# Kernel optimization log

Measured on AMD Instinct MI355X. Metric: run time of the kernel, lower is better.

## Reference

```python
import jax, jax.numpy as jnp
import numpy as np

K_CURV = 1.0   # Lorentz(k=1.0)
EPS = 1e-6


def _project(space):
    # lift space components onto hyperboloid: t = sqrt(k + ||s||^2)
    t = jnp.sqrt(K_CURV + jnp.sum(space * space, axis=-1, keepdims=True))
    return jnp.concatenate([t, space], axis=-1)


def setup_inputs():
    key = jax.random.key(0)
    B, N, D, H = 4, 1024, 128, 8
    ks = jax.random.split(key, 7)
    # valid Lorentz points: [B, N, D] with x[...,0] the time coordinate
    x = _project(jax.random.normal(ks[0], (B, N, D - 1), dtype=jnp.float32) * 0.5)
    scale = 1.0 / np.sqrt(D)
    Wq = jax.random.normal(ks[1], (H, D - 1, D), dtype=jnp.float32) * scale
    Wk = jax.random.normal(ks[2], (H, D - 1, D), dtype=jnp.float32) * scale
    Wv = jax.random.normal(ks[3], (H, D - 1, D), dtype=jnp.float32) * scale
    bq = jnp.zeros((H, D - 1), dtype=jnp.float32)
    bk = jnp.zeros((H, D - 1), dtype=jnp.float32)
    bv = jnp.zeros((H, D - 1), dtype=jnp.float32)
    beta = jnp.ones((H,), dtype=jnp.float32)
    gamma = jnp.zeros((H,), dtype=jnp.float32)
    return {"x": x, "Wq": Wq, "bq": bq, "Wk": Wk, "bk": bk, "Wv": Wv, "bv": bv,
            "beta": beta, "gamma": gamma}


def _lorentz_fc(x, W, b):
    # HyboNet-style Lorentz fully-connected (identity activation), all heads at once.
    # x: [B,N,D], W: [H,D-1,D], b: [H,D-1] -> [H,B,N,D] on the hyperboloid
    space = jnp.einsum('bnd,hed->hbne', x, W) + b[:, None, None, :]
    return _project(space)


def reference(x, Wq, bq, Wk, bk, Wv, bv, beta, gamma):
    D = x.shape[-1]
    sign = jnp.concatenate([-jnp.ones((1,), x.dtype), jnp.ones((D - 1,), x.dtype)])
    Q = _lorentz_fc(x, Wq, bq)   # [H,B,N,D]
    K = _lorentz_fc(x, Wk, bk)
    V = _lorentz_fc(x, Wv, bv)
    # pairwise Minkowski inner product <q,k>_L = -t_q t_k + s_q . s_k
    inner = jnp.einsum('hbid,hbjd->hbij', Q * sign, K)          # [H,B,N,N]
    dists = jnp.arccosh(jnp.maximum(-inner / K_CURV, 1.0 + EPS)) * np.sqrt(K_CURV)
    scores = -beta[:, None, None, None] * dists - gamma[:, None, None, None]
    attn = jax.nn.softmax(scores, axis=-1)
    # Lorentz midpoint: normalize weighted sum back onto the hyperboloid
    mid = jnp.einsum('hbij,hbjd->hbid', attn, V)                # [H,B,N,D]
    mnorm = jnp.einsum('hbid,hbid->hbi', mid * sign, mid)       # <m,m>_L (negative)
    head_out = mid * (np.sqrt(K_CURV) / jnp.sqrt(jnp.maximum(-mnorm, EPS)))[..., None]
    # direct_concat: concatenate space parts, recompute time coordinate
    H = head_out.shape[0]
    t = head_out[..., 0]                                        # [H,B,N]
    s = jnp.moveaxis(head_out[..., 1:], 0, 2)                   # [B,N,H,D-1]
    space_cat = s.reshape(s.shape[0], s.shape[1], -1)           # [B,N,H*(D-1)]
    time = jnp.sqrt(jnp.maximum(jnp.sum(t * t, axis=0) - (H - 1) * K_CURV, EPS))
    return jnp.concatenate([time[..., None], space_cat], axis=-1)  # [B,N,H*(D-1)+1]
```

## Files before the change

kernel.cpp:

```cpp
#include <hip/hip_runtime.h>

typedef __attribute__((ext_vector_type(8))) short short8_t;
typedef __attribute__((ext_vector_type(4))) short short4_t;
typedef __attribute__((ext_vector_type(4))) float float4_t;
typedef __attribute__((ext_vector_type(2))) unsigned int uint2_t;

__device__ __forceinline__ unsigned short f2bf(float f) {
    unsigned u = __builtin_bit_cast(unsigned, f);
    u += 0x7FFFu + ((u >> 16) & 1u);
    return (unsigned short)(u >> 16);
}

__device__ __forceinline__ unsigned pk_bf16(float a, float b) {
    unsigned r;
    asm("v_cvt_pk_bf16_f32 %0, %1, %2" : "=v"(r) : "v"(a), "v"(b));
    return r;
}

__device__ __forceinline__ short8_t pk8(float4_t a, float4_t b) {
    union { unsigned u[4]; short8_t s; } r;
    r.u[0] = pk_bf16(a[0], a[1]); r.u[1] = pk_bf16(a[2], a[3]);
    r.u[2] = pk_bf16(b[0], b[1]); r.u[3] = pk_bf16(b[2], b[3]);
    return r.s;
}

#define MFMA(A, B, C) __builtin_amdgcn_mfma_f32_16x16x32_bf16((A), (B), (C), 0, 0, 0)

__global__ __launch_bounds__(256, 4) void k_proj(
    const float* __restrict__ x,
    const float* __restrict__ Wq, const float* __restrict__ bq,
    const float* __restrict__ Wk, const float* __restrict__ bk,
    const float* __restrict__ Wv, const float* __restrict__ bv,
    unsigned short* __restrict__ Qs, unsigned short* __restrict__ Kb,
    unsigned short* __restrict__ Vt)
{
    __shared__ __align__(16) unsigned char lds[19456];
    unsigned short* Xs  = (unsigned short*)lds;
    unsigned short* Ot  = (unsigned short*)lds;
    unsigned short* OtT = (unsigned short*)lds;
    float*          ssqB = (float*)(lds + 18432);

    const int tid = threadIdx.x;
    const int m0  = blockIdx.x * 64;
    const int h   = blockIdx.y;
    const int mat = blockIdx.z;
    const float* W  = (mat == 0) ? Wq : ((mat == 1) ? Wk : Wv);
    const float* bb = (mat == 0) ? bq : ((mat == 1) ? bk : bv);

    const int w = tid >> 6, lane = tid & 63, li = lane & 15, lg = lane >> 4;

    const int e = w * 32 + li;
    float4_t wf[8][2];
    #pragma unroll
    for (int ni = 0; ni < 2; ni++) {
        int ee = e + ni * 16;
        const float* wp = W + (h * 127 + (ee < 127 ? ee : 0)) * 128 + lg * 8;
        #pragma unroll
        for (int kk = 0; kk < 4; kk++) {
            float4_t a = *(const float4_t*)(wp + kk * 32);
            float4_t b2 = *(const float4_t*)(wp + kk * 32 + 4);
            if (ee >= 127) { a = (float4_t){0.f,0.f,0.f,0.f}; b2 = (float4_t){0.f,0.f,0.f,0.f}; }
            wf[ni * 4 + kk][0] = a; wf[ni * 4 + kk][1] = b2;
        }
    }

    #pragma unroll
    for (int p = 0; p < 8; p++) {
        int r = p * 8 + (tid >> 5), c = (tid & 31) * 4;
        float4_t v = *(const float4_t*)(x + (m0 + r) * 128 + c);
        uint2_t u; u[0] = pk_bf16(v[0], v[1]); u[1] = pk_bf16(v[2], v[3]);
        *(uint2_t*)(Xs + r * 136 + c) = u;
    }
    __syncthreads();

    short8_t Bf[8];
    #pragma unroll
    for (int f = 0; f < 8; f++) Bf[f] = pk8(wf[f][0], wf[f][1]);

    float4_t acc[4][2];
    #pragma unroll
    for (int i = 0; i < 4; i++)
        #pragma unroll
        for (int j = 0; j < 2; j++) acc[i][j] = (float4_t){0.f, 0.f, 0.f, 0.f};

    #pragma unroll
    for (int kk = 0; kk < 4; kk++) {
        #pragma unroll
        for (int mi = 0; mi < 4; mi++) {
            short8_t A = *(short8_t*)(Xs + (mi * 16 + li) * 136 + kk * 32 + lg * 8);
            acc[mi][0] = MFMA(A, Bf[kk],     acc[mi][0]);
            acc[mi][1] = MFMA(A, Bf[4 + kk], acc[mi][1]);
        }
    }
    #pragma unroll
    for (int ni = 0; ni < 2; ni++) {
        int ee = e + ni * 16;
        float bvv = (ee < 127) ? bb[h * 127 + ee] : 0.0f;
        #pragma unroll
        for (int mi = 0; mi < 4; mi++)
            #pragma unroll
            for (int r = 0; r < 4; r++) acc[mi][ni][r] += bvv;
    }
    #pragma unroll
    for (int mi = 0; mi < 4; mi++) {
        #pragma unroll
        for (int r = 0; r < 4; r++) {
            float s = acc[mi][0][r] * acc[mi][0][r] + acc[mi][1][r] * acc[mi][1][r];
            s += __shfl_xor(s, 1);  s += __shfl_xor(s, 2);
            s += __shfl_xor(s, 4);  s += __shfl_xor(s, 8);
            if (li == 0) ssqB[(mi * 16 + lg * 4 + r) * 4 + w] = s;
        }
    }
    __syncthreads();

    if (mat < 2) {
        #pragma unroll
        for (int mi = 0; mi < 4; mi++)
            #pragma unroll
            for (int ni = 0; ni < 2; ni++) {
                int ee = e + ni * 16;
                if (ee < 127) {
                    #pragma unroll
                    for (int r = 0; r < 4; r++)
                        Ot[(mi * 16 + lg * 4 + r) * 136 + 1 + ee] = f2bf(acc[mi][ni][r]);
                }
            }
        if (tid < 64) {
            float s = ssqB[tid * 4] + ssqB[tid * 4 + 1] + ssqB[tid * 4 + 2] + ssqB[tid * 4 + 3];
            float t = sqrtf(1.0f + s);
            Ot[tid * 136] = f2bf(mat == 0 ? -t : t);
        }
        __syncthreads();
        unsigned short* dst = ((mat == 0) ? Qs : Kb) + (h * 4096 + m0) * 128;
        #pragma unroll
        for (int p = 0; p < 4; p++) {
            int r = p * 16 + (tid >> 4), c = (tid & 15) * 8;
            *(short8_t*)(dst + r * 128 + c) = *(short8_t*)(Ot + r * 136 + c);
        }
    } else {
        #pragma unroll
        for (int mi = 0; mi < 4; mi++)
            #pragma unroll
            for (int ni = 0; ni < 2; ni++) {
                int ee = e + ni * 16;
                if (ee < 127) {
                    uint2_t u;
                    u[0] = pk_bf16(acc[mi][ni][0], acc[mi][ni][1]);
                    u[1] = pk_bf16(acc[mi][ni][2], acc[mi][ni][3]);
                    *(uint2_t*)(OtT + (1 + ee) * 72 + mi * 16 + lg * 4) = u;
                }
            }
        if (tid < 64) {
            float s = ssqB[tid * 4] + ssqB[tid * 4 + 1] + ssqB[tid * 4 + 2] + ssqB[tid * 4 + 3];
            OtT[tid] = f2bf(sqrtf(1.0f + s));
        }
        __syncthreads();
        int b = m0 >> 10, n0 = m0 & 1023;
        unsigned short* dst = Vt + (h * 4 + b) * 131072 + n0;
        #pragma unroll
        for (int p = 0; p < 4; p++) {
            int d = p * 32 + (tid >> 3), nc = (tid & 7) * 8;
            *(short8_t*)(dst + d * 1024 + nc) = *(short8_t*)(OtT + d * 72 + nc);
        }
    }
}

__global__ __launch_bounds__(256, 3) void k_attn(
    const unsigned short* __restrict__ Qsg, const unsigned short* __restrict__ Kb,
    const unsigned short* __restrict__ Vt,
    const float* __restrict__ beta, const float* __restrict__ gamma,
    float* __restrict__ out, float* __restrict__ tsq)
{
    __shared__ __align__(16) unsigned char lds[45056];
    unsigned short* Ks  = (unsigned short*)lds;
    unsigned short* Vts = (unsigned short*)(lds + 17408);
    unsigned short* Ps  = (unsigned short*)(lds + 35840);
    float*          ow  = (float*)lds;

    const int tid = threadIdx.x, w = tid >> 6, lane = tid & 63;
    const int li = lane & 15, lg = lane >> 4;

    const int bid = blockIdx.x;
    const int hb = (bid & 7) * 4 + (bid >> 7);
    const int qt = (bid >> 3) & 15;
    const int h = hb >> 2, b = hb & 3;
    const int q0 = qt * 64;

    const unsigned short* Qp = Qsg + (h * 4096 + b * 1024) * 128;
    const unsigned short* Kp = Kb  + (h * 4096 + b * 1024) * 128;
    const unsigned short* Vp = Vt  + (h * 4 + b) * 131072;
    const float bet = beta[h];
    const bool beta1 = (bet == 1.0f);
    (void)gamma;

    const int kr = tid >> 4, kc = (tid & 15) * 8;
    const int vd = tid >> 3, vc = (tid & 7) * 8;
    const unsigned short* Kld = Kp + kr * 128 + kc;
    const unsigned short* Vld = Vp + vd * 1024 + vc;

    short8_t qf[4];
    const int qrow = q0 + w * 16 + li;
    #pragma unroll
    for (int kk = 0; kk < 4; kk++)
        qf[kk] = *(const short8_t*)(Qp + qrow * 128 + kk * 32 + lg * 8);

    float4_t amid[8];
    #pragma unroll
    for (int df = 0; df < 8; df++) amid[df] = (float4_t){0.f, 0.f, 0.f, 0.f};
    float m = -INFINITY, lsum = 0.0f;

    short8_t kreg[4], vreg[4];
    #pragma unroll
    for (int p = 0; p < 4; p++) {
        kreg[p] = *(const short8_t*)(Kld + p * 2048);
        vreg[p] = *(const short8_t*)(Vld + p * 32768);
    }
    #pragma unroll
    for (int p = 0; p < 4; p++) {
        *(short8_t*)(Ks  + (p * 16 + kr) * 136 + kc) = kreg[p];
        *(short8_t*)(Vts + (p * 32 + vd) * 72 + vc) = vreg[p];
    }
    __syncthreads();

    for (int t = 0; t < 16; t++) {
        if (t < 15) {
            const int j0n = (t + 1) * 64;
            #pragma unroll
            for (int p = 0; p < 4; p++) {
                kreg[p] = *(const short8_t*)(Kld + j0n * 128 + p * 2048);
                vreg[p] = *(const short8_t*)(Vld + p * 32768 + j0n);
            }
        }
        __builtin_amdgcn_sched_barrier(0);

        float4_t as[4];
        #pragma unroll
        for (int jf = 0; jf < 4; jf++) as[jf] = (float4_t){0.f, 0.f, 0.f, 0.f};
        __builtin_amdgcn_s_setprio(1);
        #pragma unroll
        for (int kk = 0; kk < 4; kk++) {
            #pragma unroll
            for (int jf = 0; jf < 4; jf++) {
                short8_t A = *(short8_t*)(Ks + (jf * 16 + li) * 136 + kk * 32 + lg * 8);
                as[jf] = MFMA(A, qf[kk], as[jf]);
            }
        }
        __builtin_amdgcn_s_setprio(0);

        float ps_ = 0.0f;
        if (beta1) {
            #pragma unroll
            for (int jf = 0; jf < 4; jf++) {
                float p[4];
                #pragma unroll
                for (int r = 0; r < 4; r++) {
                    float z = fmaxf(-as[jf][r], 1.0f + 1e-6f);
                    float wv = z + __builtin_amdgcn_sqrtf(__builtin_fmaf(z, z, -1.0f));
                    p[r] = __builtin_amdgcn_rcpf(wv);
                    ps_ += p[r];
                }
                uint2_t u; u[0] = pk_bf16(p[0], p[1]); u[1] = pk_bf16(p[2], p[3]);
                *(uint2_t*)(Ps + (w * 16 + li) * 72 + jf * 16 + lg * 4) = u;
            }
        } else {
            float s2[16];
            float tm = -INFINITY;
            #pragma unroll
            for (int jf = 0; jf < 4; jf++) {
                #pragma unroll
                for (int r = 0; r < 4; r++) {
                    float z = fmaxf(-as[jf][r], 1.0f + 1e-6f);
                    float wv = z + __builtin_amdgcn_sqrtf(__builtin_fmaf(z, z, -1.0f));
                    float s = -bet * __builtin_amdgcn_logf(wv);
                    s2[jf * 4 + r] = s;
                    tm = fmaxf(tm, s);
                }
            }
            tm = fmaxf(tm, __shfl_xor(tm, 16));
            tm = fmaxf(tm, __shfl_xor(tm, 32));
            if (__any(tm > m + 8.0f)) {
                float mn = fmaxf(m, tm);
                float scale = __builtin_amdgcn_exp2f(m - mn);
                lsum *= scale;
                #pragma unroll
                for (int df = 0; df < 8; df++)
                    #pragma unroll
                    for (int r = 0; r < 4; r++) amid[df][r] *= scale;
                m = mn;
            }
            #pragma unroll
            for (int jf = 0; jf < 4; jf++) {
                float p0 = __builtin_amdgcn_exp2f(s2[jf * 4 + 0] - m);
                float p1 = __builtin_amdgcn_exp2f(s2[jf * 4 + 1] - m);
                float p2 = __builtin_amdgcn_exp2f(s2[jf * 4 + 2] - m);
                float p3 = __builtin_amdgcn_exp2f(s2[jf * 4 + 3] - m);
                ps_ += (p0 + p1) + (p2 + p3);
                uint2_t u; u[0] = pk_bf16(p0, p1); u[1] = pk_bf16(p2, p3);
                *(uint2_t*)(Ps + (w * 16 + li) * 72 + jf * 16 + lg * 4) = u;
            }
        }
        ps_ += __shfl_xor(ps_, 16);
        ps_ += __shfl_xor(ps_, 32);
        lsum += ps_;
        asm volatile("s_waitcnt lgkmcnt(0)" ::: "memory");
        __builtin_amdgcn_sched_barrier(0);

        __builtin_amdgcn_s_setprio(1);
        #pragma unroll
        for (int kk2 = 0; kk2 < 2; kk2++) {
            short8_t Bp = *(short8_t*)(Ps + (w * 16 + li) * 72 + kk2 * 32 + lg * 8);
            #pragma unroll
            for (int df = 0; df < 8; df++) {
                short8_t A = *(short8_t*)(Vts + (df * 16 + li) * 72 + kk2 * 32 + lg * 8);
                amid[df] = MFMA(A, Bp, amid[df]);
            }
        }
        __builtin_amdgcn_s_setprio(0);

        if (t < 15) {
            __syncthreads();
            #pragma unroll
            for (int p = 0; p < 4; p++) {
                *(short8_t*)(Ks  + (p * 16 + kr) * 136 + kc) = kreg[p];
                *(short8_t*)(Vts + (p * 32 + vd) * 72 + vc) = vreg[p];
            }
            __syncthreads();
        }
    }

    float invl = 1.0f / lsum;
    float ssq = 0.0f;
    #pragma unroll
    for (int df = 0; df < 8; df++) {
        #pragma unroll
        for (int r = 0; r < 4; r++) {
            float v = amid[df][r] * invl;
            amid[df][r] = v;
            ssq += v * v;
        }
    }
    ssq += __shfl_xor(ssq, 16);
    ssq += __shfl_xor(ssq, 32);
    float tmid = __shfl(amid[0][0], li);
    float denom = fmaxf(2.0f * tmid * tmid - ssq, 1e-6f);
    float rs = 1.0f / sqrtf(denom);

    __syncthreads();
    #pragma unroll
    for (int df = 0; df < 8; df++) {
        #pragma unroll
        for (int r = 0; r < 4; r++)
            ow[w * 2112 + li * 132 + df * 16 + lg * 4 + r] = amid[df][r] * rs;
    }
    asm volatile("s_waitcnt lgkmcnt(0)" ::: "memory");
    __builtin_amdgcn_sched_barrier(0);

    #pragma unroll
    for (int i = 0; i < 16; i++) {
        int n = q0 + w * 16 + i;
        float v0 = ow[w * 2112 + i * 132 + lane];
        float v1 = ow[w * 2112 + i * 132 + 64 + lane];
        float* orow = out + (b * 1024 + n) * 1017;
        if (lane == 0) tsq[h * 4096 + b * 1024 + n] = v0 * v0;
        else           orow[h * 127 + lane] = v0;
        orow[h * 127 + 64 + lane] = v1;
    }
}

__global__ __launch_bounds__(256) void k_time(const float* __restrict__ tsq,
                                              float* __restrict__ out)
{
    int mrow = blockIdx.x * 256 + threadIdx.x;
    float s = 0.0f;
    #pragma unroll
    for (int h = 0; h < 8; h++) s += tsq[h * 4096 + mrow];
    out[mrow * 1017] = sqrtf(fmaxf(s - 7.0f, 1e-6f));
}

extern "C" void kernel_launch(void* const* d_in, const int* in_sizes, int n_in,
                              void* d_out, int out_size, void* d_ws, size_t ws_size,
                              hipStream_t stream)
{
    const float* x    = (const float*)d_in[0];
    const float* Wq   = (const float*)d_in[1];
    const float* bq   = (const float*)d_in[2];
    const float* Wk   = (const float*)d_in[3];
    const float* bk   = (const float*)d_in[4];
    const float* Wv   = (const float*)d_in[5];
    const float* bv   = (const float*)d_in[6];
    const float* beta = (const float*)d_in[7];
    const float* gam  = (const float*)d_in[8];
    float* out = (float*)d_out;

    unsigned char* ws = (unsigned char*)d_ws;
    unsigned short* Qs = (unsigned short*)(ws);
    unsigned short* Kb = (unsigned short*)(ws + 8388608);
    unsigned short* Vt = (unsigned short*)(ws + 16777216);
    float*          ts = (float*)(ws + 25165824);

    k_proj<<<dim3(64, 8, 3), 256, 0, stream>>>(x, Wq, bq, Wk, bk, Wv, bv, Qs, Kb, Vt);
    k_attn<<<dim3(512), 256, 0, stream>>>(Qs, Kb, Vt, beta, gam, out, ts);
    k_time<<<dim3(16), 256, 0, stream>>>(ts, out);
}
```

Baseline: 137.8 us.

## Split attention over key halves with partial outputs merged in separate kernel

Each attention block now handles half of the key sequence, which doubles the grid from 512 to 1024 blocks. Blocks write unnormalized partial accumulators and the running max to a workspace, and a new merge kernel combines the two halves, normalizes onto the hyperboloid and computes the time coordinate. The running sum is dropped, because the Lorentz renormalization makes the softmax denominator cancel. LDS tiles switch from padded rows to an XOR-swizzled layout, which shrinks LDS enough to raise occupancy to 4 blocks per CU, at the cost of extra partial-buffer traffic and one more launch.

```diff
diff --git a/kernel.cpp b/kernel.cpp
--- a/kernel.cpp
+++ b/kernel.cpp
@@ -165,24 +165,25 @@
     }
 }
 
-__global__ __launch_bounds__(256, 3) void k_attn(
+__global__ __launch_bounds__(256, 4) void k_attn(
     const unsigned short* __restrict__ Qsg, const unsigned short* __restrict__ Kb,
     const unsigned short* __restrict__ Vt,
     const float* __restrict__ beta, const float* __restrict__ gamma,
-    float* __restrict__ out, float* __restrict__ tsq)
+    float* __restrict__ part)
 {
-    __shared__ __align__(16) unsigned char lds[45056];
-    unsigned short* Ks  = (unsigned short*)lds;
-    unsigned short* Vts = (unsigned short*)(lds + 17408);
-    unsigned short* Ps  = (unsigned short*)(lds + 35840);
-    float*          ow  = (float*)lds;
+    __shared__ __align__(16) unsigned char lds[40960];
+    char* Kl = (char*)lds;
+    char* Vl = (char*)lds + 16384;
+    char* Pl = (char*)lds + 32768;
+    float* pw = (float*)lds;
 
     const int tid = threadIdx.x, w = tid >> 6, lane = tid & 63;
     const int li = lane & 15, lg = lane >> 4;
 
     const int bid = blockIdx.x;
-    const int hb = (bid & 7) * 4 + (bid >> 7);
-    const int qt = (bid >> 3) & 15;
+    const int hb = bid & 31;
+    const int qt = (bid >> 5) & 15;
+    const int half = (bid >> 9) & 1;
     const int h = hb >> 2, b = hb & 3;
     const int q0 = qt * 64;
 
@@ -193,10 +194,18 @@
     const bool beta1 = (bet == 1.0f);
     (void)gamma;
 
-    const int kr = tid >> 4, kc = (tid & 15) * 8;
-    const int vd = tid >> 3, vc = (tid & 7) * 8;
-    const unsigned short* Kld = Kp + kr * 128 + kc;
-    const unsigned short* Vld = Vp + vd * 1024 + vc;
+    const int kr = tid >> 4, kc16 = (tid & 15) * 16;
+    const int vd = tid >> 3, vc16 = (tid & 7) * 16;
+    const int kwb = (kr * 256 + kc16) ^ ((kr & 7) << 4);
+    const int vwb = (vd * 128 + vc16) ^ ((vd & 7) << 4);
+    const unsigned short* Kld = Kp + (half * 512 + kr) * 128 + (tid & 15) * 8;
+    const unsigned short* Vld = Vp + vd * 1024 + half * 512 + (tid & 7) * 8;
+
+    const int lxor = (li & 7) << 4;
+    const int krb = (li * 256 + lg * 16) ^ lxor;
+    const int vrb = (li * 128 + lg * 16) ^ lxor;
+    const int prb = ((w * 16 + li) * 128 + lg * 16) ^ lxor;
+    const int pwb = ((w * 16 + li) * 128 + lg * 8) ^ lxor;
 
     short8_t qf[4];
     const int qrow = q0 + w * 16 + li;
@@ -207,7 +216,7 @@
     float4_t amid[8];
     #pragma unroll
     for (int df = 0; df < 8; df++) amid[df] = (float4_t){0.f, 0.f, 0.f, 0.f};
-    float m = -INFINITY, lsum = 0.0f;
+    float m = beta1 ? 0.0f : -INFINITY;
 
     short8_t kreg[4], vreg[4];
     #pragma unroll
@@ -217,13 +226,13 @@
     }
     #pragma unroll
     for (int p = 0; p < 4; p++) {
-        *(short8_t*)(Ks  + (p * 16 + kr) * 136 + kc) = kreg[p];
-        *(short8_t*)(Vts + (p * 32 + vd) * 72 + vc) = vreg[p];
+        *(short8_t*)(Kl + p * 4096 + kwb) = kreg[p];
+        *(short8_t*)(Vl + p * 4096 + vwb) = vreg[p];
     }
     __syncthreads();
 
-    for (int t = 0; t < 16; t++) {
-        if (t < 15) {
+    for (int t = 0; t < 8; t++) {
+        if (t < 7) {
             const int j0n = (t + 1) * 64;
             #pragma unroll
             for (int p = 0; p < 4; p++) {
@@ -241,13 +250,12 @@
         for (int kk = 0; kk < 4; kk++) {
             #pragma unroll
             for (int jf = 0; jf < 4; jf++) {
-                short8_t A = *(short8_t*)(Ks + (jf * 16 + li) * 136 + kk * 32 + lg * 8);
+                short8_t A = *(short8_t*)(Kl + ((jf * 4096 + kk * 64) ^ krb));
                 as[jf] = MFMA(A, qf[kk], as[jf]);
             }
         }
         __builtin_amdgcn_s_setprio(0);
 
-        float ps_ = 0.0f;
         if (beta1) {
             #pragma unroll
             for (int jf = 0; jf < 4; jf++) {
@@ -257,10 +265,9 @@
                     float z = fmaxf(-as[jf][r], 1.0f + 1e-6f);
                     float wv = z + __builtin_amdgcn_sqrtf(__builtin_fmaf(z, z, -1.0f));
                     p[r] = __builtin_amdgcn_rcpf(wv);
-                    ps_ += p[r];
                 }
                 uint2_t u; u[0] = pk_bf16(p[0], p[1]); u[1] = pk_bf16(p[2], p[3]);
-                *(uint2_t*)(Ps + (w * 16 + li) * 72 + jf * 16 + lg * 4) = u;
+                *(uint2_t*)(Pl + ((jf * 32) ^ pwb)) = u;
             }
         } else {
             float s2[16];
@@ -281,7 +288,6 @@
             if (__any(tm > m + 8.0f)) {
                 float mn = fmaxf(m, tm);
                 float scale = __builtin_amdgcn_exp2f(m - mn);
-                lsum *= scale;
                 #pragma unroll
                 for (int df = 0; df < 8; df++)
                     #pragma unroll
@@ -294,87 +300,113 @@
                 float p1 = __builtin_amdgcn_exp2f(s2[jf * 4 + 1] - m);
                 float p2 = __builtin_amdgcn_exp2f(s2[jf * 4 + 2] - m);
                 float p3 = __builtin_amdgcn_exp2f(s2[jf * 4 + 3] - m);
-                ps_ += (p0 + p1) + (p2 + p3);
                 uint2_t u; u[0] = pk_bf16(p0, p1); u[1] = pk_bf16(p2, p3);
-                *(uint2_t*)(Ps + (w * 16 + li) * 72 + jf * 16 + lg * 4) = u;
-            }
-        }
-        ps_ += __shfl_xor(ps_, 16);
-        ps_ += __shfl_xor(ps_, 32);
-        lsum += ps_;
+                *(uint2_t*)(Pl + ((jf * 32) ^ pwb)) = u;
+            }
+        }
         asm volatile("s_waitcnt lgkmcnt(0)" ::: "memory");
         __builtin_amdgcn_sched_barrier(0);
 
         __builtin_amdgcn_s_setprio(1);
         #pragma unroll
         for (int kk2 = 0; kk2 < 2; kk2++) {
-            short8_t Bp = *(short8_t*)(Ps + (w * 16 + li) * 72 + kk2 * 32 + lg * 8);
+            short8_t Bp = *(short8_t*)(Pl + ((kk2 * 64) ^ prb));
             #pragma unroll
             for (int df = 0; df < 8; df++) {
-                short8_t A = *(short8_t*)(Vts + (df * 16 + li) * 72 + kk2 * 32 + lg * 8);
+                short8_t A = *(short8_t*)(Vl + ((df * 2048 + kk2 * 64) ^ vrb));
                 amid[df] = MFMA(A, Bp, amid[df]);
             }
         }
         __builtin_amdgcn_s_setprio(0);
 
-        if (t < 15) {
+        if (t < 7) {
             __syncthreads();
             #pragma unroll
             for (int p = 0; p < 4; p++) {
-                *(short8_t*)(Ks  + (p * 16 + kr) * 136 + kc) = kreg[p];
-                *(short8_t*)(Vts + (p * 32 + vd) * 72 + vc) = vreg[p];
+                *(short8_t*)(Kl + p * 4096 + kwb) = kreg[p];
+                *(short8_t*)(Vl + p * 4096 + vwb) = vreg[p];
             }
             __syncthreads();
         }
     }
 
-    float invl = 1.0f / lsum;
-    float ssq = 0.0f;
+    __syncthreads();
     #pragma unroll
     for (int df = 0; df < 8; df++) {
         #pragma unroll
-        for (int r = 0; r < 4; r++) {
-            float v = amid[df][r] * invl;
-            amid[df][r] = v;
-            ssq += v * v;
-        }
-    }
-    ssq += __shfl_xor(ssq, 16);
-    ssq += __shfl_xor(ssq, 32);
-    float tmid = __shfl(amid[0][0], li);
-    float denom = fmaxf(2.0f * tmid * tmid - ssq, 1e-6f);
-    float rs = 1.0f / sqrtf(denom);
-
-    __syncthreads();
-    #pragma unroll
-    for (int df = 0; df < 8; df++) {
-        #pragma unroll
         for (int r = 0; r < 4; r++)
-            ow[w * 2112 + li * 132 + df * 16 + lg * 4 + r] = amid[df][r] * rs;
-    }
+            pw[w * 2112 + li * 132 + df * 16 + lg * 4 + r] = amid[df][r];
+    }
+    if (lg == 0) pw[w * 2112 + li * 132 + 128] = m;
     asm volatile("s_waitcnt lgkmcnt(0)" ::: "memory");
     __builtin_amdgcn_sched_barrier(0);
 
-    #pragma unroll
-    for (int i = 0; i < 16; i++) {
-        int n = q0 + w * 16 + i;
-        float v0 = ow[w * 2112 + i * 132 + lane];
-        float v1 = ow[w * 2112 + i * 132 + 64 + lane];
-        float* orow = out + (b * 1024 + n) * 1017;
-        if (lane == 0) tsq[h * 4096 + b * 1024 + n] = v0 * v0;
-        else           orow[h * 127 + lane] = v0;
-        orow[h * 127 + 64 + lane] = v1;
-    }
-}
-
-__global__ __launch_bounds__(256) void k_time(const float* __restrict__ tsq,
-                                              float* __restrict__ out)
+    float* pb = part + (size_t)(((half * 8 + h) * 4 + b) * 1024 + q0 + w * 16) * 132;
+    #pragma unroll
+    for (int it = 0; it < 8; it++) {
+        int idx = it * 64 + lane;
+        int row = idx >> 5, c4 = idx & 31;
+        *(float4_t*)(pb + row * 132 + c4 * 4) =
+            *(float4_t*)(pw + w * 2112 + row * 132 + c4 * 4);
+    }
+    if (lane < 16)
+        *(float4_t*)(pb + lane * 132 + 128) =
+            *(float4_t*)(pw + w * 2112 + lane * 132 + 128);
+}
+
+__global__ __launch_bounds__(256) void k_merge(const float* __restrict__ part,
+                                               float* __restrict__ out)
 {
-    int mrow = blockIdx.x * 256 + threadIdx.x;
-    float s = 0.0f;
-    #pragma unroll
-    for (int h = 0; h < 8; h++) s += tsq[h * 4096 + mrow];
-    out[mrow * 1017] = sqrtf(fmaxf(s - 7.0f, 1e-6f));
+    const int tid = threadIdx.x, w = tid >> 6, lane = tid & 63;
+    const int h = lane >> 3, sub = lane & 7;
+    const int row = blockIdx.x * 4 + w;
+    const int b = row >> 10, n = row & 1023;
+
+    const float* p0 = part + (size_t)(((0 * 8 + h) * 4 + b) * 1024 + n) * 132;
+    const float* p1 = part + (size_t)(((1 * 8 + h) * 4 + b) * 1024 + n) * 132;
+
+    float4_t a0[4], a1[4];
+    #pragma unroll
+    for (int q = 0; q < 4; q++) {
+        a0[q] = *(const float4_t*)(p0 + sub * 16 + q * 4);
+        a1[q] = *(const float4_t*)(p1 + sub * 16 + q * 4);
+    }
+    float m0 = p0[128], m1 = p1[128];
+    float mN = fmaxf(m0, m1);
+    float s0 = __builtin_amdgcn_exp2f(m0 - mN);
+    float s1 = __builtin_amdgcn_exp2f(m1 - mN);
+
+    float4_t acc[4];
+    float ssq = 0.0f;
+    #pragma unroll
+    for (int q = 0; q < 4; q++) {
+        #pragma unroll
+        for (int e2 = 0; e2 < 4; e2++) {
+            float v = a0[q][e2] * s0 + a1[q][e2] * s1;
+            acc[q][e2] = v;
+            ssq += v * v;
+        }
+    }
+    ssq += __shfl_xor(ssq, 1);
+    ssq += __shfl_xor(ssq, 2);
+    ssq += __shfl_xor(ssq, 4);
+    float t = __shfl(acc[0][0], lane & 56);
+    float denom = fmaxf(2.0f * t * t - ssq, 1e-6f);
+    float rs = 1.0f / sqrtf(denom);
+
+    float th2 = (t * rs) * (t * rs);
+    th2 += __shfl_xor(th2, 8);
+    th2 += __shfl_xor(th2, 16);
+    th2 += __shfl_xor(th2, 32);
+    float timec = sqrtf(fmaxf(th2 - 7.0f, 1e-6f));
+
+    float* orow = out + (size_t)row * 1017;
+    if (lane == 0) orow[0] = timec;
+    #pragma unroll
+    for (int k = 0; k < 16; k++) {
+        int d = sub * 16 + k;
+        if (d > 0) orow[h * 127 + d] = acc[k >> 2][k & 3] * rs;
+    }
 }
 
 extern "C" void kernel_launch(void* const* d_in, const int* in_sizes, int n_in,
@@ -396,9 +428,9 @@
     unsigned short* Qs = (unsigned short*)(ws);
     unsigned short* Kb = (unsigned short*)(ws + 8388608);
     unsigned short* Vt = (unsigned short*)(ws + 16777216);
-    float*          ts = (float*)(ws + 25165824);
+    float*          pt = (float*)(ws + 25165824);
 
     k_proj<<<dim3(64, 8, 3), 256, 0, stream>>>(x, Wq, bq, Wk, bk, Wv, bv, Qs, Kb, Vt);
-    k_attn<<<dim3(512), 256, 0, stream>>>(Qs, Kb, Vt, beta, gam, out, ts);
-    k_time<<<dim3(16), 256, 0, stream>>>(ts, out);
-}
+    k_attn<<<dim3(1024), 256, 0, stream>>>(Qs, Kb, Vt, beta, gam, pt);
+    k_merge<<<dim3(1024), 256, 0, stream>>>(pt, out);
+}
```

Result: slower. 256.4 us (+86.0%).

## Split attention KV range across two wave groups with XOR-swizzled LDS

Applied to the files above, without the earlier changes.

The attention kernel doubles its block to 512 threads: two groups of four waves each process half of the key/value sequence for the same 64 queries, and their partial midpoint accumulators are merged through LDS at the end. The LDS tiles for K, V and P are rewritten with XOR swizzling in place of padding, to avoid bank conflicts. The running softmax sum lsum is dropped, relying on the final Lorentz normalization being scale invariant. The trade-offs are larger LDS use per block (80 KB), a merge step, and a lower clamp epsilon on the normalization denominator.

```diff
diff --git a/kernel.cpp b/kernel.cpp
--- a/kernel.cpp
+++ b/kernel.cpp
@@ -165,25 +165,25 @@
     }
 }
 
-__global__ __launch_bounds__(256, 3) void k_attn(
+__global__ __launch_bounds__(512, 4) void k_attn(
     const unsigned short* __restrict__ Qsg, const unsigned short* __restrict__ Kb,
     const unsigned short* __restrict__ Vt,
     const float* __restrict__ beta, const float* __restrict__ gamma,
     float* __restrict__ out, float* __restrict__ tsq)
 {
-    __shared__ __align__(16) unsigned char lds[45056];
-    unsigned short* Ks  = (unsigned short*)lds;
-    unsigned short* Vts = (unsigned short*)(lds + 17408);
-    unsigned short* Ps  = (unsigned short*)(lds + 35840);
-    float*          ow  = (float*)lds;
+    __shared__ __align__(16) unsigned char lds[81920];
+    char*  L   = (char*)lds;
+    float* mrg = (float*)lds;
+    float* ow  = (float*)(lds + 34816);
 
     const int tid = threadIdx.x, w = tid >> 6, lane = tid & 63;
     const int li = lane & 15, lg = lane >> 4;
+    const int qsub = w & 3, half = w >> 2;
 
     const int bid = blockIdx.x;
-    const int hb = (bid & 7) * 4 + (bid >> 7);
+    const int h = bid & 7;
     const int qt = (bid >> 3) & 15;
-    const int h = hb >> 2, b = hb & 3;
+    const int b = bid >> 7;
     const int q0 = qt * 64;
 
     const unsigned short* Qp = Qsg + (h * 4096 + b * 1024) * 128;
@@ -193,13 +193,22 @@
     const bool beta1 = (bet == 1.0f);
     (void)gamma;
 
-    const int kr = tid >> 4, kc = (tid & 15) * 8;
-    const int vd = tid >> 3, vc = (tid & 7) * 8;
-    const unsigned short* Kld = Kp + kr * 128 + kc;
-    const unsigned short* Vld = Vp + vd * 1024 + vc;
+    const int hv = tid >> 8, s = tid & 255;
+    const int kr = s >> 4, kcl = s & 15;
+    const int vd = s >> 3, vcl = s & 7;
+    const unsigned short* Kld = Kp + (hv * 512 + kr) * 128 + kcl * 8;
+    const unsigned short* Vld = Vp + vd * 1024 + hv * 512 + vcl * 8;
+    const int kwb = hv * 16384 + ((kr * 256 + kcl * 16) ^ ((kr & 7) << 4));
+    const int vwb = 32768 + hv * 16384 + ((vd * 128 + vcl * 16) ^ ((vd & 7) << 4));
+
+    const int lxor = (li & 7) << 4;
+    const int krb = half * 16384 + ((li * 256 + lg * 16) ^ lxor);
+    const int vrb = 32768 + half * 16384 + ((li * 128 + lg * 16) ^ lxor);
+    const int pwb = 65536 + w * 2048 + ((li * 128 + lg * 8) ^ lxor);
+    const int prb = 65536 + w * 2048 + ((li * 128 + lg * 16) ^ lxor);
 
     short8_t qf[4];
-    const int qrow = q0 + w * 16 + li;
+    const int qrow = q0 + qsub * 16 + li;
     #pragma unroll
     for (int kk = 0; kk < 4; kk++)
         qf[kk] = *(const short8_t*)(Qp + qrow * 128 + kk * 32 + lg * 8);
@@ -207,7 +216,7 @@
     float4_t amid[8];
     #pragma unroll
     for (int df = 0; df < 8; df++) amid[df] = (float4_t){0.f, 0.f, 0.f, 0.f};
-    float m = -INFINITY, lsum = 0.0f;
+    float m = beta1 ? 0.0f : -INFINITY;
 
     short8_t kreg[4], vreg[4];
     #pragma unroll
@@ -217,18 +226,17 @@
     }
     #pragma unroll
     for (int p = 0; p < 4; p++) {
-        *(short8_t*)(Ks  + (p * 16 + kr) * 136 + kc) = kreg[p];
-        *(short8_t*)(Vts + (p * 32 + vd) * 72 + vc) = vreg[p];
+        *(short8_t*)(L + kwb + p * 4096) = kreg[p];
+        *(short8_t*)(L + vwb + p * 4096) = vreg[p];
     }
     __syncthreads();
 
-    for (int t = 0; t < 16; t++) {
-        if (t < 15) {
-            const int j0n = (t + 1) * 64;
+    for (int t = 0; t < 8; t++) {
+        if (t < 7) {
             #pragma unroll
             for (int p = 0; p < 4; p++) {
-                kreg[p] = *(const short8_t*)(Kld + j0n * 128 + p * 2048);
-                vreg[p] = *(const short8_t*)(Vld + p * 32768 + j0n);
+                kreg[p] = *(const short8_t*)(Kld + (t + 1) * 8192 + p * 2048);
+                vreg[p] = *(const short8_t*)(Vld + p * 32768 + (t + 1) * 64);
             }
         }
         __builtin_amdgcn_sched_barrier(0);
@@ -241,13 +249,12 @@
         for (int kk = 0; kk < 4; kk++) {
             #pragma unroll
             for (int jf = 0; jf < 4; jf++) {
-                short8_t A = *(short8_t*)(Ks + (jf * 16 + li) * 136 + kk * 32 + lg * 8);
+                short8_t A = *(short8_t*)(L + ((jf * 4096 + kk * 64) ^ krb));
                 as[jf] = MFMA(A, qf[kk], as[jf]);
             }
         }
         __builtin_amdgcn_s_setprio(0);
 
-        float ps_ = 0.0f;
         if (beta1) {
             #pragma unroll
             for (int jf = 0; jf < 4; jf++) {
@@ -257,10 +264,9 @@
                     float z = fmaxf(-as[jf][r], 1.0f + 1e-6f);
                     float wv = z + __builtin_amdgcn_sqrtf(__builtin_fmaf(z, z, -1.0f));
                     p[r] = __builtin_amdgcn_rcpf(wv);
-                    ps_ += p[r];
                 }
                 uint2_t u; u[0] = pk_bf16(p[0], p[1]); u[1] = pk_bf16(p[2], p[3]);
-                *(uint2_t*)(Ps + (w * 16 + li) * 72 + jf * 16 + lg * 4) = u;
+                *(uint2_t*)(L + ((jf * 32) ^ pwb)) = u;
             }
         } else {
             float s2[16];
@@ -271,9 +277,9 @@
                 for (int r = 0; r < 4; r++) {
                     float z = fmaxf(-as[jf][r], 1.0f + 1e-6f);
                     float wv = z + __builtin_amdgcn_sqrtf(__builtin_fmaf(z, z, -1.0f));
-                    float s = -bet * __builtin_amdgcn_logf(wv);
-                    s2[jf * 4 + r] = s;
-                    tm = fmaxf(tm, s);
+                    float sc = -bet * __builtin_amdgcn_logf(wv);
+                    s2[jf * 4 + r] = sc;
+                    tm = fmaxf(tm, sc);
                 }
             }
             tm = fmaxf(tm, __shfl_xor(tm, 16));
@@ -281,7 +287,6 @@
             if (__any(tm > m + 8.0f)) {
                 float mn = fmaxf(m, tm);
                 float scale = __builtin_amdgcn_exp2f(m - mn);
-                lsum *= scale;
                 #pragma unroll
                 for (int df = 0; df < 8; df++)
                     #pragma unroll
@@ -294,72 +299,95 @@
                 float p1 = __builtin_amdgcn_exp2f(s2[jf * 4 + 1] - m);
                 float p2 = __builtin_amdgcn_exp2f(s2[jf * 4 + 2] - m);
                 float p3 = __builtin_amdgcn_exp2f(s2[jf * 4 + 3] - m);
-                ps_ += (p0 + p1) + (p2 + p3);
                 uint2_t u; u[0] = pk_bf16(p0, p1); u[1] = pk_bf16(p2, p3);
-                *(uint2_t*)(Ps + (w * 16 + li) * 72 + jf * 16 + lg * 4) = u;
-            }
-        }
-        ps_ += __shfl_xor(ps_, 16);
-        ps_ += __shfl_xor(ps_, 32);
-        lsum += ps_;
+                *(uint2_t*)(L + ((jf * 32) ^ pwb)) = u;
+            }
+        }
         asm volatile("s_waitcnt lgkmcnt(0)" ::: "memory");
         __builtin_amdgcn_sched_barrier(0);
 
         __builtin_amdgcn_s_setprio(1);
         #pragma unroll
         for (int kk2 = 0; kk2 < 2; kk2++) {
-            short8_t Bp = *(short8_t*)(Ps + (w * 16 + li) * 72 + kk2 * 32 + lg * 8);
+            short8_t Bp = *(short8_t*)(L + ((kk2 * 64) ^ prb));
             #pragma unroll
             for (int df = 0; df < 8; df++) {
-                short8_t A = *(short8_t*)(Vts + (df * 16 + li) * 72 + kk2 * 32 + lg * 8);
+                short8_t A = *(short8_t*)(L + ((df * 2048 + kk2 * 64) ^ vrb));
                 amid[df] = MFMA(A, Bp, amid[df]);
             }
         }
         __builtin_amdgcn_s_setprio(0);
 
-        if (t < 15) {
+        if (t < 7) {
             __syncthreads();
             #pragma unroll
             for (int p = 0; p < 4; p++) {
-                *(short8_t*)(Ks  + (p * 16 + kr) * 136 + kc) = kreg[p];
-                *(short8_t*)(Vts + (p * 32 + vd) * 72 + vc) = vreg[p];
+                *(short8_t*)(L + kwb + p * 4096) = kreg[p];
+                *(short8_t*)(L + vwb + p * 4096) = vreg[p];
             }
             __syncthreads();
         }
     }
 
-    float invl = 1.0f / lsum;
+    __syncthreads();
+    if (half == 1) {
+        float* mb = mrg + qsub * 2112;
+        #pragma unroll
+        for (int df = 0; df < 8; df++)
+            #pragma unroll
+            for (int r = 0; r < 4; r++)
+                mb[li * 132 + df * 16 + lg * 4 + r] = amid[df][r];
+        if (lg == 0) mb[li * 132 + 128] = m;
+    }
+    __syncthreads();
+    if (half == 1) return;
+
+    {
+        float* mb = mrg + qsub * 2112;
+        if (beta1) {
+            #pragma unroll
+            for (int df = 0; df < 8; df++)
+                #pragma unroll
+                for (int r = 0; r < 4; r++)
+                    amid[df][r] += mb[li * 132 + df * 16 + lg * 4 + r];
+        } else {
+            float m1v = mb[li * 132 + 128];
+            float mN = fmaxf(m, m1v);
+            float s0 = __builtin_amdgcn_exp2f(m - mN);
+            float s1 = __builtin_amdgcn_exp2f(m1v - mN);
+            #pragma unroll
+            for (int df = 0; df < 8; df++)
+                #pragma unroll
+                for (int r = 0; r < 4; r++)
+                    amid[df][r] = amid[df][r] * s0 + mb[li * 132 + df * 16 + lg * 4 + r] * s1;
+        }
+    }
+
     float ssq = 0.0f;
     #pragma unroll
-    for (int df = 0; df < 8; df++) {
-        #pragma unroll
-        for (int r = 0; r < 4; r++) {
-            float v = amid[df][r] * invl;
-            amid[df][r] = v;
-            ssq += v * v;
-        }
-    }
+    for (int df = 0; df < 8; df++)
+        #pragma unroll
+        for (int r = 0; r < 4; r++) ssq += amid[df][r] * amid[df][r];
     ssq += __shfl_xor(ssq, 16);
     ssq += __shfl_xor(ssq, 32);
     float tmid = __shfl(amid[0][0], li);
-    float denom = fmaxf(2.0f * tmid * tmid - ssq, 1e-6f);
+    float denom = fmaxf(2.0f * tmid * tmid - ssq, 1e-12f);
     float rs = 1.0f / sqrtf(denom);
 
-    __syncthreads();
     #pragma unroll
     for (int df = 0; df < 8; df++) {
         #pragma unroll
         for (int r = 0; r < 4; r++)
-            ow[w * 2112 + li * 132 + df * 16 + lg * 4 + r] = amid[df][r] * rs;
+            ow[qsub * 2112 + li * 132 + df * 16 + lg * 4 + r] = amid[df][r] * rs;
     }
     asm volatile("s_waitcnt lgkmcnt(0)" ::: "memory");
     __builtin_amdgcn_sched_barrier(0);
 
     #pragma unroll
     for (int i = 0; i < 16; i++) {
-        int n = q0 + w * 16 + i;
-        float v0 = ow[w * 2112 + i * 132 + lane];
-        float v1 = ow[w * 2112 + i * 132 + 64 + lane];
+        int n = q0 + qsub * 16 + i;
+        float v0 = ow[qsub * 2112 + i * 132 + lane];
+        float v1 = ow[qsub * 2112 + i * 132 + 64 + lane];
         float* orow = out + (b * 1024 + n) * 1017;
         if (lane == 0) tsq[h * 4096 + b * 1024 + n] = v0 * v0;
         else           orow[h * 127 + lane] = v0;
@@ -399,6 +427,6 @@
     float*          ts = (float*)(ws + 25165824);
 
     k_proj<<<dim3(64, 8, 3), 256, 0, stream>>>(x, Wq, bq, Wk, bk, Wv, bv, Qs, Kb, Vt);
-    k_attn<<<dim3(512), 256, 0, stream>>>(Qs, Kb, Vt, beta, gam, out, ts);
+    k_attn<<<dim3(512), 512, 0, stream>>>(Qs, Kb, Vt, beta, gam, out, ts);
     k_time<<<dim3(16), 256, 0, stream>>>(ts, out);
 }
```

New measurement: 163.2 us. 1.18x slower.
